# Performance work log

Hardware: AMD Instinct MI355X
Metric: run time of the kernel (lower is better)

The kernel has to match this reference:

```python
import jax, jax.numpy as jnp
import numpy as np

B, S, D, H = 4, 2048, 768, 12
DEPTH = D // H


def setup_inputs() -> dict:
    key = jax.random.key(0)
    ks = jax.random.split(key, 8)
    scale = 1.0 / np.sqrt(D)
    return {
        "v": jax.random.normal(ks[0], (B, S, D), jnp.float32),
        "k": jax.random.normal(ks[1], (B, S, D), jnp.float32),
        "q": jax.random.normal(ks[2], (B, S, D), jnp.float32),
        "wq": jax.random.normal(ks[3], (D, D), jnp.float32) * scale,
        "wk": jax.random.normal(ks[4], (D, D), jnp.float32) * scale,
        "wv": jax.random.normal(ks[5], (D, D), jnp.float32) * scale,
        "wo": jax.random.normal(ks[6], (D, D), jnp.float32) * scale,
        "bo": jax.random.normal(ks[7], (D,), jnp.float32) * 0.01,
    }


def _split_heads(x):
    # [B, S, D] -> [B, H, S, depth]
    return x.reshape(B, S, H, DEPTH).transpose(0, 2, 1, 3)


def reference(v, k, q, wq, wk, wv, wo, bo):
    # nn.Linear(bias=False): y = x @ W.T
    qh = _split_heads(q @ wq.T)
    kh = _split_heads(k @ wk.T)
    vh = _split_heads(v @ wv.T)
    # scaled dot-product attention (mask=None)
    logits = jnp.einsum("bhqd,bhkd->bhqk", qh, kh) / jnp.sqrt(
        jnp.asarray(DEPTH, jnp.float32)
    )
    attn = jax.nn.softmax(logits, axis=-1)  # [B, H, Sq, Sk]
    out = jnp.einsum("bhqk,bhkd->bhqd", attn, vh)
    concat = out.transpose(0, 2, 1, 3).reshape(B, S, D)
    return concat @ wo.T + bo
```

## Files before the change

### kernel.cpp

```cpp
#include <hip/hip_runtime.h>
#include <math.h>

#define BB 4
#define SS 2048
#define DD 768
#define HH 12
#define DEPTH 64
#define M_TOTAL (BB * SS)
#define WSZ (DD * DD)

typedef __attribute__((ext_vector_type(8))) short bf16x8;
typedef __attribute__((ext_vector_type(16))) float f32x16;
typedef __attribute__((ext_vector_type(4))) float f32x4;
typedef __attribute__((ext_vector_type(4))) unsigned short us4;
typedef __attribute__((ext_vector_type(2))) unsigned int u32x2;
typedef __attribute__((ext_vector_type(4))) unsigned int u32x4;

__device__ __forceinline__ unsigned short f2b(float f) {
  unsigned u = __builtin_bit_cast(unsigned, f);
  return (unsigned short)((u + 0x8000u) >> 16);
}

__device__ __forceinline__ unsigned pkrnd(float lo, float hi) {
  unsigned a = __builtin_bit_cast(unsigned, lo) + 0x8000u;
  unsigned b = __builtin_bit_cast(unsigned, hi) + 0x8000u;
  return __builtin_amdgcn_perm(b, a, 0x07060302);
}

__device__ __forceinline__ us4 f2b4(float a, float b, float c, float d) {
  unsigned lo = pkrnd(a, b), hi = pkrnd(c, d);
  us4 t;
  t.x = (unsigned short)lo; t.y = (unsigned short)(lo >> 16);
  t.z = (unsigned short)hi; t.w = (unsigned short)(hi >> 16);
  return t;
}

__device__ __forceinline__ unsigned cvtpk(float a, float b) {
  unsigned d;
  asm("v_cvt_pk_bf16_f32 %0, %1, %2" : "=v"(d) : "v"(a), "v"(b));
  return d;
}

__device__ __forceinline__ u32x2 permswap(unsigned a, unsigned b) {
  auto r = __builtin_amdgcn_permlane32_swap(a, b, false, false);
  u32x2 out;
  out.x = r[0];
  out.y = r[1];
  return out;
}

__device__ __forceinline__ float fexp2(float x) {
  return __builtin_amdgcn_exp2f(x);
}

__device__ __forceinline__ void gl16(const void* g, void* l) {
  __builtin_amdgcn_global_load_lds(
      (const __attribute__((address_space(1))) unsigned int*)g,
      (__attribute__((address_space(3))) unsigned int*)l, 16, 0, 0);
}

__global__ __launch_bounds__(256) void prep(
    const float* __restrict__ s0, const float* __restrict__ s1,
    const float* __restrict__ s2, const float* __restrict__ s3,
    const float* __restrict__ s4, const float* __restrict__ s5,
    const float* __restrict__ s6, unsigned short* __restrict__ d0,
    unsigned short* __restrict__ d1, unsigned short* __restrict__ d2,
    unsigned short* __restrict__ d3, unsigned short* __restrict__ d4,
    unsigned short* __restrict__ d5, unsigned short* __restrict__ d6) {
  const float* s;
  unsigned short* d;
  int n;
  switch (blockIdx.y) {
    case 0: s = s0; d = d0; n = M_TOTAL * DD; break;
    case 1: s = s1; d = d1; n = M_TOTAL * DD; break;
    case 2: s = s2; d = d2; n = M_TOTAL * DD; break;
    case 3: s = s3; d = d3; n = WSZ; break;
    case 4: s = s4; d = d4; n = WSZ; break;
    case 5: s = s5; d = d5; n = WSZ; break;
    default: s = s6; d = d6; n = WSZ; break;
  }
  int idx = (blockIdx.x * 256 + threadIdx.x) * 4;
  if (idx >= n) return;
  float4 f = *(const float4*)(s + idx);
  *(us4*)(d + idx) = f2b4(f.x, f.y, f.z, f.w);
}

__global__ __launch_bounds__(256) void proj_qkv(
    const unsigned short* __restrict__ qb, const unsigned short* __restrict__ kb,
    const unsigned short* __restrict__ vb, const unsigned short* __restrict__ wqb,
    const unsigned short* __restrict__ wkb, const unsigned short* __restrict__ wvb,
    unsigned short* __restrict__ QF, unsigned short* __restrict__ KF,
    unsigned short* __restrict__ VF) {
  const int mode = blockIdx.z;
  const unsigned short* X;
  const unsigned short* W;
  if (mode == 0) { X = qb; W = wqb; }
  else if (mode == 1) { X = kb; W = wkb; }
  else { X = vb; W = wvb; }

  __shared__ __align__(16) char sm[34816];
  unsigned short* As = (unsigned short*)sm;
  unsigned short* Bs = (unsigned short*)(sm + 8192);
  unsigned short* Ts = (unsigned short*)sm;

  const int tid = threadIdx.x;
  const int lane = tid & 63, w_ = tid >> 6;
  const int lr = lane & 15, quad = lane >> 4;
  const int wm = (w_ & 1) * 64, wn = (w_ >> 1) * 64;
  const int lin = blockIdx.y * 64 + blockIdx.x;
  const int nlin = (lin & 7) * 48 + (lin >> 3);
  const int m0 = (nlin / 6) * 128, n0 = (nlin % 6) * 128;
  const int grow = lane >> 2, gcol = (lane & 3) * 8;

  f32x4 acc[4][4];
#pragma unroll
  for (int mt = 0; mt < 4; ++mt)
#pragma unroll
    for (int nt = 0; nt < 4; ++nt) acc[mt][nt] = (f32x4){0.f, 0.f, 0.f, 0.f};

  for (int k0 = 0; k0 < DD; k0 += 32) {
    __syncthreads();
#pragma unroll
    for (int i = 0; i < 2; ++i) {
      int c = 4 * i + w_;
      int row = c * 16 + grow;
      gl16(X + (size_t)(m0 + row) * DD + k0 + gcol, (char*)As + c * 1024);
      gl16(W + (size_t)(n0 + row) * DD + k0 + gcol, (char*)Bs + c * 1024);
    }
    __syncthreads();

    bf16x8 af[4];
#pragma unroll
    for (int mt = 0; mt < 4; ++mt)
      af[mt] = *(const bf16x8*)&As[(wm + 16 * mt + lr) * 32 + 8 * quad];
#pragma unroll
    for (int nt = 0; nt < 4; ++nt) {
      bf16x8 bf = *(const bf16x8*)&Bs[(wn + 16 * nt + lr) * 32 + 8 * quad];
#pragma unroll
      for (int mt = 0; mt < 4; ++mt)
        acc[mt][nt] = __builtin_amdgcn_mfma_f32_16x16x32_bf16(af[mt], bf,
                                                              acc[mt][nt], 0, 0, 0);
    }
  }

  __syncthreads();

  const int b_ = m0 >> 11;
  const int hbase = n0 >> 6;
  const int sgbase = (m0 & 2047) >> 5;

  if (mode < 2) {
    const float osc = (mode == 0) ? 0.18033688011f : 1.0f;
#pragma unroll
    for (int mt = 0; mt < 4; ++mt)
#pragma unroll
      for (int nt = 0; nt < 4; ++nt) {
        int n = wn + 16 * nt + lr;
        int mb = wm + 16 * mt + 4 * quad;
#pragma unroll
        for (int r = 0; r < 4; ++r)
          Ts[(mb + r) * 136 + n] = f2b(acc[mt][nt][r] * osc);
      }
    __syncthreads();
    unsigned short* O = (mode == 0) ? QF : KF;
    const int ks = tid >> 6, lane2 = tid & 63;
    const int mrow = lane2 & 31, hb = lane2 >> 5;
#pragma unroll
    for (int c = 0; c < 8; ++c) {
      int hl = c >> 2, sblk = c & 3;
      int bh = b_ * HH + hbase + hl;
      bf16x8 vv = *(const bf16x8*)&Ts[(sblk * 32 + mrow) * 136 + hl * 64 +
                                      ks * 16 + hb * 8];
      *(bf16x8*)(O + ((size_t)bh * 64 + sgbase + sblk) * 2048 + tid * 8) = vv;
    }
  } else {
#pragma unroll
    for (int mt = 0; mt < 4; ++mt)
#pragma unroll
      for (int nt = 0; nt < 4; ++nt) {
        int n = wn + 16 * nt + lr;
        int mb = wm + 16 * mt + 4 * quad;
        *(us4*)&Ts[n * 136 + mb] =
            f2b4(acc[mt][nt][0], acc[mt][nt][1], acc[mt][nt][2], acc[mt][nt][3]);
      }
    __syncthreads();
    const int ntv = tid >> 7, ks2 = (tid >> 6) & 1, lane2 = tid & 63;
#pragma unroll
    for (int c = 0; c < 8; ++c) {
      int hl = c >> 2, sblk = c & 3;
      int bh = b_ * HH + hbase + hl;
      bf16x8 vv = *(const bf16x8*)&Ts[(hl * 64 + ntv * 32 + (lane2 & 31)) * 136 +
                                      sblk * 32 + ks2 * 16 + (lane2 >> 5) * 8];
      *(bf16x8*)(VF + ((size_t)bh * 64 + sgbase + sblk) * 2048 + tid * 8) = vv;
    }
  }
}

struct KV {
  bf16x8 k[4];
  bf16x8 v[4];
};

__global__ __launch_bounds__(256) void attn(
    const unsigned short* __restrict__ QF, const unsigned short* __restrict__ KF,
    const unsigned short* __restrict__ VF, unsigned short* __restrict__ cc) {
  __shared__ __align__(16) char smem[19200];
  float (*Osh)[64][36] = (float (*)[64][36])smem;
  float (*Ls)[2][32] = (float (*)[2][32])(smem + 18432);
  float (*Linv)[32] = (float (*)[32])(smem + 18944);

  const int tid = threadIdx.x;
  const int lane = tid & 63, w_ = tid >> 6;
  const int wq = w_ & 1, wk = w_ >> 1;
  const int m32 = lane & 31, h = lane >> 5;
  const int lin = blockIdx.y * 32 + blockIdx.x;
  const int nlin = (lin & 7) * 192 + (lin >> 3);
  const int bh = nlin >> 5;
  const int q0 = (nlin & 31) * 64;
  const size_t perbh = (size_t)SS * DEPTH;

  const unsigned short* qfb = QF + (size_t)bh * perbh;
  const unsigned short* kfb = KF + (size_t)bh * perbh + (size_t)wk * 2048 + lane * 8;
  const unsigned short* vfb = VF + (size_t)bh * perbh + (size_t)wk * 2048 + lane * 8;

  bf16x8 qf[4];
  {
    const unsigned short* p = qfb + (size_t)((q0 >> 5) + wq) * 2048 + lane * 8;
#pragma unroll
    for (int ks = 0; ks < 4; ++ks) qf[ks] = *(const bf16x8*)(p + ks * 512);
  }

  f32x16 o[2];
#pragma unroll
  for (int nt = 0; nt < 2; ++nt)
#pragma unroll
    for (int r = 0; r < 16; ++r) o[nt][r] = 0.f;
  float l_lane = 0.f;

#define LOADKV(tile, dst)                                                    \
  do {                                                                       \
    const unsigned short* kp_ = kfb + (size_t)(tile) * 4096;                 \
    const unsigned short* vp_ = vfb + (size_t)(tile) * 4096;                 \
    _Pragma("unroll") for (int x_ = 0; x_ < 4; ++x_) {                       \
      (dst).k[x_] = *(const bf16x8*)(kp_ + x_ * 512);                        \
      (dst).v[x_] = *(const bf16x8*)(vp_ + x_ * 512);                        \
    }                                                                        \
  } while (0)

#define QKCOMP(kv, st)                                                       \
  do {                                                                       \
    _Pragma("unroll") for (int r_ = 0; r_ < 16; ++r_) (st)[r_] = 0.f;        \
    __builtin_amdgcn_s_setprio(1);                                           \
    _Pragma("unroll") for (int ks_ = 0; ks_ < 4; ++ks_)                      \
        (st) = __builtin_amdgcn_mfma_f32_32x32x16_bf16((kv).k[ks_], qf[ks_], \
                                                       (st), 0, 0, 0);       \
    __builtin_amdgcn_s_setprio(0);                                           \
  } while (0)

#define EXPPV(st, kv)                                                        \
  do {                                                                       \
    float e_[16];                                                            \
    _Pragma("unroll") for (int r_ = 0; r_ < 16; ++r_) e_[r_] = fexp2((st)[r_]); \
    _Pragma("unroll") for (int g_ = 0; g_ < 4; ++g_)                         \
        l_lane += (e_[4 * g_ + 0] + e_[4 * g_ + 1]) +                        \
                  (e_[4 * g_ + 2] + e_[4 * g_ + 3]);                         \
    unsigned w00 = cvtpk(e_[0], e_[1]), w01 = cvtpk(e_[2], e_[3]);           \
    unsigned w10 = cvtpk(e_[4], e_[5]), w11 = cvtpk(e_[6], e_[7]);           \
    unsigned w20 = cvtpk(e_[8], e_[9]), w21 = cvtpk(e_[10], e_[11]);         \
    unsigned w30 = cvtpk(e_[12], e_[13]), w31 = cvtpk(e_[14], e_[15]);       \
    u32x2 r0 = permswap(w00, w10);                                           \
    u32x2 r1 = permswap(w01, w11);                                           \
    u32x2 r2 = permswap(w20, w30);                                           \
    u32x2 r3 = permswap(w21, w31);                                           \
    u32x4 paw0, paw1;                                                        \
    paw0.x = r0.x; paw0.y = r1.x; paw0.z = r0.y; paw0.w = r1.y;              \
    paw1.x = r2.x; paw1.y = r3.x; paw1.z = r2.y; paw1.w = r3.y;              \
    bf16x8 pa0 = __builtin_bit_cast(bf16x8, paw0);                           \
    bf16x8 pa1 = __builtin_bit_cast(bf16x8, paw1);                           \
    __builtin_amdgcn_s_setprio(1);                                           \
    o[0] = __builtin_amdgcn_mfma_f32_32x32x16_bf16(pa0, (kv).v[0], o[0],     \
                                                   0, 0, 0);                 \
    o[1] = __builtin_amdgcn_mfma_f32_32x32x16_bf16(pa0, (kv).v[2], o[1],     \
                                                   0, 0, 0);                 \
    o[0] = __builtin_amdgcn_mfma_f32_32x32x16_bf16(pa1, (kv).v[1], o[0],     \
                                                   0, 0, 0);                 \
    o[1] = __builtin_amdgcn_mfma_f32_32x32x16_bf16(pa1, (kv).v[3], o[1],     \
                                                   0, 0, 0);                 \
    __builtin_amdgcn_s_setprio(0);                                           \
  } while (0)

  KV b0, b1;
  f32x16 st0, st1;
  LOADKV(0, b0);
  LOADKV(1, b1);
  for (int t = 0; t < 32; t += 2) {
    QKCOMP(b0, st0);
    QKCOMP(b1, st1);
    EXPPV(st0, b0);
    if (t + 2 < 32) LOADKV(t + 2, b0);
    EXPPV(st1, b1);
    if (t + 3 < 32) LOADKV(t + 3, b1);
  }

  l_lane += __shfl_xor(l_lane, 32);
  if (h == 0) Ls[wq][wk][m32] = l_lane;
  __syncthreads();
  if (wk == 1) {
#pragma unroll
    for (int nt = 0; nt < 2; ++nt)
#pragma unroll
      for (int g = 0; g < 4; ++g) {
        float4 t = make_float4(o[nt][4 * g], o[nt][4 * g + 1], o[nt][4 * g + 2],
                               o[nt][4 * g + 3]);
        *(float4*)&Osh[wq][32 * nt + m32][8 * g + 4 * h] = t;
      }
  } else if (tid < 64) {
    int qq = tid & 31, ww = tid >> 5;
    Linv[ww][qq] = 1.f / (Ls[ww][0][qq] + Ls[ww][1][qq]);
  }
  __syncthreads();
  if (wk == 0) {
    const int b_ = bh / HH, h_ = bh % HH;
#pragma unroll
    for (int g = 0; g < 4; ++g) {
      float4 li = *(const float4*)&Linv[wq][8 * g + 4 * h];
      float lia[4] = {li.x, li.y, li.z, li.w};
#pragma unroll
      for (int nt = 0; nt < 2; ++nt) {
        float4 ot = *(const float4*)&Osh[wq][32 * nt + m32][8 * g + 4 * h];
        float oa[4] = {ot.x, ot.y, ot.z, ot.w};
#pragma unroll
        for (int r = 0; r < 4; ++r) {
          int qg = q0 + 32 * wq + 8 * g + 4 * h + r;
          float val = (o[nt][4 * g + r] + oa[r]) * lia[r];
          cc[((size_t)b_ * SS + qg) * DD + h_ * DEPTH + 32 * nt + m32] = f2b(val);
        }
      }
    }
  }
}

__global__ __launch_bounds__(256) void proj_out(
    const unsigned short* __restrict__ cc, const unsigned short* __restrict__ wob,
    const float* __restrict__ bo, float* __restrict__ out) {
  __shared__ __align__(16) unsigned short As[128 * 32];
  __shared__ __align__(16) unsigned short Bs[128 * 32];

  const int tid = threadIdx.x;
  const int lane = tid & 63, w_ = tid >> 6;
  const int lr = lane & 15, quad = lane >> 4;
  const int wm = (w_ & 1) * 64, wn = (w_ >> 1) * 64;
  const int lin = blockIdx.y * 64 + blockIdx.x;
  const int nlin = (lin & 7) * 48 + (lin >> 3);
  const int m0 = (nlin / 6) * 128, n0 = (nlin % 6) * 128;
  const int grow = lane >> 2, gcol = (lane & 3) * 8;

  f32x4 acc[4][4];
#pragma unroll
  for (int mt = 0; mt < 4; ++mt)
#pragma unroll
    for (int nt = 0; nt < 4; ++nt) acc[mt][nt] = (f32x4){0.f, 0.f, 0.f, 0.f};

  for (int k0 = 0; k0 < DD; k0 += 32) {
    __syncthreads();
#pragma unroll
    for (int i = 0; i < 2; ++i) {
      int c = 4 * i + w_;
      int row = c * 16 + grow;
      gl16(cc + (size_t)(m0 + row) * DD + k0 + gcol, (char*)As + c * 1024);
      gl16(wob + (size_t)(n0 + row) * DD + k0 + gcol, (char*)Bs + c * 1024);
    }
    __syncthreads();

    bf16x8 af[4];
#pragma unroll
    for (int mt = 0; mt < 4; ++mt)
      af[mt] = *(const bf16x8*)&As[(wm + 16 * mt + lr) * 32 + 8 * quad];
#pragma unroll
    for (int nt = 0; nt < 4; ++nt) {
      bf16x8 bf = *(const bf16x8*)&Bs[(wn + 16 * nt + lr) * 32 + 8 * quad];
#pragma unroll
      for (int mt = 0; mt < 4; ++mt)
        acc[mt][nt] = __builtin_amdgcn_mfma_f32_16x16x32_bf16(af[mt], bf,
                                                              acc[mt][nt], 0, 0, 0);
    }
  }

#pragma unroll
  for (int mt = 0; mt < 4; ++mt)
#pragma unroll
    for (int nt = 0; nt < 4; ++nt) {
      int n = n0 + wn + 16 * nt + lr;
      float bias = bo[n];
#pragma unroll
      for (int r = 0; r < 4; ++r) {
        int m = m0 + wm + 16 * mt + 4 * quad + r;
        out[(size_t)m * DD + n] = acc[mt][nt][r] + bias;
      }
    }
}

extern "C" void kernel_launch(void* const* d_in, const int* in_sizes, int n_in,
                              void* d_out, int out_size, void* d_ws,
                              size_t ws_size, hipStream_t stream) {
  const float* v = (const float*)d_in[0];
  const float* k = (const float*)d_in[1];
  const float* q = (const float*)d_in[2];
  const float* wq = (const float*)d_in[3];
  const float* wk = (const float*)d_in[4];
  const float* wv = (const float*)d_in[5];
  const float* wo = (const float*)d_in[6];
  const float* bo = (const float*)d_in[7];
  float* out = (float*)d_out;

  const size_t per = (size_t)BB * HH * SS * DEPTH;
  unsigned short* QF = (unsigned short*)d_ws;
  unsigned short* KF = QF + per;
  unsigned short* VF = KF + per;
  unsigned short* cc = VF + per;
  unsigned short* qb = cc + per;
  unsigned short* kb = qb + per;
  unsigned short* vb = kb + per;
  unsigned short* wqb = vb + per;
  unsigned short* wkb = wqb + WSZ;
  unsigned short* wvb = wkb + WSZ;
  unsigned short* wob = wvb + WSZ;

  dim3 g0(M_TOTAL * DD / 1024, 7);
  prep<<<g0, 256, 0, stream>>>(q, k, v, wq, wk, wv, wo, qb, kb, vb, wqb, wkb,
                               wvb, wob);

  dim3 g1(M_TOTAL / 128, DD / 128, 3);
  proj_qkv<<<g1, 256, 0, stream>>>(qb, kb, vb, wqb, wkb, wvb, QF, KF, VF);

  dim3 g2(SS / 64, BB * HH);
  attn<<<g2, 256, 0, stream>>>(QF, KF, VF, cc);

  dim3 g3(M_TOTAL / 128, DD / 128);
  proj_out<<<g3, 256, 0, stream>>>(cc, wob, bo, out);
}
```

Baseline: 271.0 us.

## Double attention query tile per block and compact prep launch grid

The attention kernel now handles 128 queries per block instead of 64. Each wave keeps two 32-row query fragments, so every K/V tile loaded into registers feeds twice as many MFMAs, which halves K/V global traffic per query. The cost is more registers, shared memory doubled to about 38 KB, and half as many blocks. Separately, the prep conversion kernel moves from a 2D grid, where many blocks exited early for the small weight matrices, to a 1D grid sized exactly to the data, which removes the idle blocks.

Result: slower. 276.7 us (+2.1%).

```diff
diff --git a/kernel.cpp b/kernel.cpp
--- a/kernel.cpp
+++ b/kernel.cpp
@@ -69,18 +69,23 @@
     unsigned short* __restrict__ d5, unsigned short* __restrict__ d6) {
   const float* s;
   unsigned short* d;
-  int n;
-  switch (blockIdx.y) {
-    case 0: s = s0; d = d0; n = M_TOTAL * DD; break;
-    case 1: s = s1; d = d1; n = M_TOTAL * DD; break;
-    case 2: s = s2; d = d2; n = M_TOTAL * DD; break;
-    case 3: s = s3; d = d3; n = WSZ; break;
-    case 4: s = s4; d = d4; n = WSZ; break;
-    case 5: s = s5; d = d5; n = WSZ; break;
-    default: s = s6; d = d6; n = WSZ; break;
-  }
-  int idx = (blockIdx.x * 256 + threadIdx.x) * 4;
-  if (idx >= n) return;
+  int b = blockIdx.x, lb;
+  if (b < 18432) {
+    int mode = b / 6144;
+    lb = b - mode * 6144;
+    if (mode == 0) { s = s0; d = d0; }
+    else if (mode == 1) { s = s1; d = d1; }
+    else { s = s2; d = d2; }
+  } else {
+    int t = b - 18432;
+    int mode = t / 576;
+    lb = t - mode * 576;
+    if (mode == 0) { s = s3; d = d3; }
+    else if (mode == 1) { s = s4; d = d4; }
+    else if (mode == 2) { s = s5; d = d5; }
+    else { s = s6; d = d6; }
+  }
+  int idx = (lb * 256 + threadIdx.x) * 4;
   float4 f = *(const float4*)(s + idx);
   *(us4*)(d + idx) = f2b4(f.x, f.y, f.z, f.w);
 }
@@ -204,38 +209,42 @@
 __global__ __launch_bounds__(256) void attn(
     const unsigned short* __restrict__ QF, const unsigned short* __restrict__ KF,
     const unsigned short* __restrict__ VF, unsigned short* __restrict__ cc) {
-  __shared__ __align__(16) char smem[19200];
-  float (*Osh)[64][36] = (float (*)[64][36])smem;
-  float (*Ls)[2][32] = (float (*)[2][32])(smem + 18432);
-  float (*Linv)[32] = (float (*)[32])(smem + 18944);
+  __shared__ __align__(16) char smem[38400];
+  float (*Osh)[2][64][36] = (float (*)[2][64][36])smem;
+  float (*Ls)[2][2][32] = (float (*)[2][2][32])(smem + 36864);
+  float (*Linv)[2][32] = (float (*)[2][32])(smem + 37888);
 
   const int tid = threadIdx.x;
   const int lane = tid & 63, w_ = tid >> 6;
   const int wq = w_ & 1, wk = w_ >> 1;
   const int m32 = lane & 31, h = lane >> 5;
-  const int lin = blockIdx.y * 32 + blockIdx.x;
-  const int nlin = (lin & 7) * 192 + (lin >> 3);
-  const int bh = nlin >> 5;
-  const int q0 = (nlin & 31) * 64;
+  const int lin = blockIdx.y * 16 + blockIdx.x;
+  const int nlin = (lin & 7) * 96 + (lin >> 3);
+  const int bh = nlin >> 4;
+  const int q0 = (nlin & 15) * 128;
   const size_t perbh = (size_t)SS * DEPTH;
 
   const unsigned short* qfb = QF + (size_t)bh * perbh;
   const unsigned short* kfb = KF + (size_t)bh * perbh + (size_t)wk * 2048 + lane * 8;
   const unsigned short* vfb = VF + (size_t)bh * perbh + (size_t)wk * 2048 + lane * 8;
 
-  bf16x8 qf[4];
+  bf16x8 qf0[4], qf1[4];
   {
-    const unsigned short* p = qfb + (size_t)((q0 >> 5) + wq) * 2048 + lane * 8;
-#pragma unroll
-    for (int ks = 0; ks < 4; ++ks) qf[ks] = *(const bf16x8*)(p + ks * 512);
-  }
-
-  f32x16 o[2];
+    const unsigned short* p0 =
+        qfb + (size_t)((q0 >> 5) + 2 * wq) * 2048 + lane * 8;
+#pragma unroll
+    for (int ks = 0; ks < 4; ++ks) {
+      qf0[ks] = *(const bf16x8*)(p0 + ks * 512);
+      qf1[ks] = *(const bf16x8*)(p0 + 2048 + ks * 512);
+    }
+  }
+
+  f32x16 o0[2], o1[2];
 #pragma unroll
   for (int nt = 0; nt < 2; ++nt)
 #pragma unroll
-    for (int r = 0; r < 16; ++r) o[nt][r] = 0.f;
-  float l_lane = 0.f;
+    for (int r = 0; r < 16; ++r) { o0[nt][r] = 0.f; o1[nt][r] = 0.f; }
+  float l0 = 0.f, l1 = 0.f;
 
 #define LOADKV(tile, dst)                                                    \
   do {                                                                       \
@@ -247,23 +256,13 @@
     }                                                                        \
   } while (0)
 
-#define QKCOMP(kv, st)                                                       \
-  do {                                                                       \
-    _Pragma("unroll") for (int r_ = 0; r_ < 16; ++r_) (st)[r_] = 0.f;        \
-    __builtin_amdgcn_s_setprio(1);                                           \
-    _Pragma("unroll") for (int ks_ = 0; ks_ < 4; ++ks_)                      \
-        (st) = __builtin_amdgcn_mfma_f32_32x32x16_bf16((kv).k[ks_], qf[ks_], \
-                                                       (st), 0, 0, 0);       \
-    __builtin_amdgcn_s_setprio(0);                                           \
-  } while (0)
-
-#define EXPPV(st, kv)                                                        \
+#define EXPPV(st, kv, oo, ll)                                                \
   do {                                                                       \
     float e_[16];                                                            \
     _Pragma("unroll") for (int r_ = 0; r_ < 16; ++r_) e_[r_] = fexp2((st)[r_]); \
     _Pragma("unroll") for (int g_ = 0; g_ < 4; ++g_)                         \
-        l_lane += (e_[4 * g_ + 0] + e_[4 * g_ + 1]) +                        \
-                  (e_[4 * g_ + 2] + e_[4 * g_ + 3]);                         \
+        (ll) += (e_[4 * g_ + 0] + e_[4 * g_ + 1]) +                          \
+                (e_[4 * g_ + 2] + e_[4 * g_ + 3]);                           \
     unsigned w00 = cvtpk(e_[0], e_[1]), w01 = cvtpk(e_[2], e_[3]);           \
     unsigned w10 = cvtpk(e_[4], e_[5]), w11 = cvtpk(e_[6], e_[7]);           \
     unsigned w20 = cvtpk(e_[8], e_[9]), w21 = cvtpk(e_[10], e_[11]);         \
@@ -278,62 +277,93 @@
     bf16x8 pa0 = __builtin_bit_cast(bf16x8, paw0);                           \
     bf16x8 pa1 = __builtin_bit_cast(bf16x8, paw1);                           \
     __builtin_amdgcn_s_setprio(1);                                           \
-    o[0] = __builtin_amdgcn_mfma_f32_32x32x16_bf16(pa0, (kv).v[0], o[0],     \
-                                                   0, 0, 0);                 \
-    o[1] = __builtin_amdgcn_mfma_f32_32x32x16_bf16(pa0, (kv).v[2], o[1],     \
-                                                   0, 0, 0);                 \
-    o[0] = __builtin_amdgcn_mfma_f32_32x32x16_bf16(pa1, (kv).v[1], o[0],     \
-                                                   0, 0, 0);                 \
-    o[1] = __builtin_amdgcn_mfma_f32_32x32x16_bf16(pa1, (kv).v[3], o[1],     \
-                                                   0, 0, 0);                 \
+    (oo)[0] = __builtin_amdgcn_mfma_f32_32x32x16_bf16(pa0, (kv).v[0],        \
+                                                      (oo)[0], 0, 0, 0);     \
+    (oo)[1] = __builtin_amdgcn_mfma_f32_32x32x16_bf16(pa0, (kv).v[2],        \
+                                                      (oo)[1], 0, 0, 0);     \
+    (oo)[0] = __builtin_amdgcn_mfma_f32_32x32x16_bf16(pa1, (kv).v[1],        \
+                                                      (oo)[0], 0, 0, 0);     \
+    (oo)[1] = __builtin_amdgcn_mfma_f32_32x32x16_bf16(pa1, (kv).v[3],        \
+                                                      (oo)[1], 0, 0, 0);     \
     __builtin_amdgcn_s_setprio(0);                                           \
   } while (0)
 
+#define TILE2(kv)                                                            \
+  do {                                                                       \
+    f32x16 st0, st1;                                                         \
+    _Pragma("unroll") for (int r_ = 0; r_ < 16; ++r_) {                      \
+      st0[r_] = 0.f; st1[r_] = 0.f;                                          \
+    }                                                                        \
+    __builtin_amdgcn_s_setprio(1);                                           \
+    _Pragma("unroll") for (int ks_ = 0; ks_ < 4; ++ks_)                      \
+        st0 = __builtin_amdgcn_mfma_f32_32x32x16_bf16((kv).k[ks_], qf0[ks_], \
+                                                      st0, 0, 0, 0);         \
+    _Pragma("unroll") for (int ks_ = 0; ks_ < 4; ++ks_)                      \
+        st1 = __builtin_amdgcn_mfma_f32_32x32x16_bf16((kv).k[ks_], qf1[ks_], \
+                                                      st1, 0, 0, 0);         \
+    __builtin_amdgcn_s_setprio(0);                                           \
+    EXPPV(st0, kv, o0, l0);                                                  \
+    EXPPV(st1, kv, o1, l1);                                                  \
+  } while (0)
+
   KV b0, b1;
-  f32x16 st0, st1;
   LOADKV(0, b0);
   LOADKV(1, b1);
   for (int t = 0; t < 32; t += 2) {
-    QKCOMP(b0, st0);
-    QKCOMP(b1, st1);
-    EXPPV(st0, b0);
+    TILE2(b0);
     if (t + 2 < 32) LOADKV(t + 2, b0);
-    EXPPV(st1, b1);
+    TILE2(b1);
     if (t + 3 < 32) LOADKV(t + 3, b1);
   }
 
-  l_lane += __shfl_xor(l_lane, 32);
-  if (h == 0) Ls[wq][wk][m32] = l_lane;
+  l0 += __shfl_xor(l0, 32);
+  l1 += __shfl_xor(l1, 32);
+  if (h == 0) {
+    Ls[wq][0][wk][m32] = l0;
+    Ls[wq][1][wk][m32] = l1;
+  }
   __syncthreads();
   if (wk == 1) {
 #pragma unroll
     for (int nt = 0; nt < 2; ++nt)
 #pragma unroll
       for (int g = 0; g < 4; ++g) {
-        float4 t = make_float4(o[nt][4 * g], o[nt][4 * g + 1], o[nt][4 * g + 2],
-                               o[nt][4 * g + 3]);
-        *(float4*)&Osh[wq][32 * nt + m32][8 * g + 4 * h] = t;
+        float4 t0 = make_float4(o0[nt][4 * g], o0[nt][4 * g + 1],
+                                o0[nt][4 * g + 2], o0[nt][4 * g + 3]);
+        float4 t1 = make_float4(o1[nt][4 * g], o1[nt][4 * g + 1],
+                                o1[nt][4 * g + 2], o1[nt][4 * g + 3]);
+        *(float4*)&Osh[wq][0][32 * nt + m32][8 * g + 4 * h] = t0;
+        *(float4*)&Osh[wq][1][32 * nt + m32][8 * g + 4 * h] = t1;
       }
-  } else if (tid < 64) {
-    int qq = tid & 31, ww = tid >> 5;
-    Linv[ww][qq] = 1.f / (Ls[ww][0][qq] + Ls[ww][1][qq]);
+  } else {
+    int qq = tid & 31, qg_ = (tid >> 5) & 1, wq_ = tid >> 6;
+    Linv[wq_][qg_][qq] =
+        1.f / (Ls[wq_][qg_][0][qq] + Ls[wq_][qg_][1][qq]);
   }
   __syncthreads();
   if (wk == 0) {
     const int b_ = bh / HH, h_ = bh % HH;
 #pragma unroll
     for (int g = 0; g < 4; ++g) {
-      float4 li = *(const float4*)&Linv[wq][8 * g + 4 * h];
-      float lia[4] = {li.x, li.y, li.z, li.w};
+      float4 li0 = *(const float4*)&Linv[wq][0][8 * g + 4 * h];
+      float4 li1 = *(const float4*)&Linv[wq][1][8 * g + 4 * h];
+      float l0a[4] = {li0.x, li0.y, li0.z, li0.w};
+      float l1a[4] = {li1.x, li1.y, li1.z, li1.w};
 #pragma unroll
       for (int nt = 0; nt < 2; ++nt) {
-        float4 ot = *(const float4*)&Osh[wq][32 * nt + m32][8 * g + 4 * h];
-        float oa[4] = {ot.x, ot.y, ot.z, ot.w};
+        float4 p0 = *(const float4*)&Osh[wq][0][32 * nt + m32][8 * g + 4 * h];
+        float4 p1 = *(const float4*)&Osh[wq][1][32 * nt + m32][8 * g + 4 * h];
+        float o0a[4] = {p0.x, p0.y, p0.z, p0.w};
+        float o1a[4] = {p1.x, p1.y, p1.z, p1.w};
 #pragma unroll
         for (int r = 0; r < 4; ++r) {
-          int qg = q0 + 32 * wq + 8 * g + 4 * h + r;
-          float val = (o[nt][4 * g + r] + oa[r]) * lia[r];
-          cc[((size_t)b_ * SS + qg) * DD + h_ * DEPTH + 32 * nt + m32] = f2b(val);
+          int qbase = q0 + 64 * wq + 8 * g + 4 * h + r;
+          float v0 = (o0[nt][4 * g + r] + o0a[r]) * l0a[r];
+          float v1 = (o1[nt][4 * g + r] + o1a[r]) * l1a[r];
+          cc[((size_t)b_ * SS + qbase) * DD + h_ * DEPTH + 32 * nt + m32] =
+              f2b(v0);
+          cc[((size_t)b_ * SS + qbase + 32) * DD + h_ * DEPTH + 32 * nt + m32] =
+              f2b(v1);
         }
       }
     }
@@ -426,14 +456,13 @@
   unsigned short* wvb = wkb + WSZ;
   unsigned short* wob = wvb + WSZ;
 
-  dim3 g0(M_TOTAL * DD / 1024, 7);
-  prep<<<g0, 256, 0, stream>>>(q, k, v, wq, wk, wv, wo, qb, kb, vb, wqb, wkb,
-                               wvb, wob);
+  prep<<<dim3(20736), 256, 0, stream>>>(q, k, v, wq, wk, wv, wo, qb, kb, vb,
+                                        wqb, wkb, wvb, wob);
 
   dim3 g1(M_TOTAL / 128, DD / 128, 3);
   proj_qkv<<<g1, 256, 0, stream>>>(qb, kb, vb, wqb, wkb, wvb, QF, KF, VF);
 
-  dim3 g2(SS / 64, BB * HH);
+  dim3 g2(SS / 128, BB * HH);
   attn<<<g2, 256, 0, stream>>>(QF, KF, VF, cc);
 
   dim3 g3(M_TOTAL / 128, DD / 128);
```

## Fuse fp32-to-bf16 conversion of q/k/v into the QKV projection GEMM

Applied to the files above, without the earlier changes.

The prep kernel no longer converts the large q/k/v activations to bf16. It now converts only the four weight matrices, using a flattened 1D grid. The QKV projection kernel instead loads fp32 activation rows directly, rounds them to bf16 in registers and writes them to shared memory, while weights still use async global-to-LDS loads. This removes a full write and re-read of three bf16 activation copies. In exchange, the GEMM reads fp32 (twice the bytes) and redoes each conversion once for every N-tile column (6 times), with synchronous register staging in place of async LDS loads.

Result: slower. 293.0 us (+8.1%).

```diff
diff --git a/kernel.cpp b/kernel.cpp
--- a/kernel.cpp
+++ b/kernel.cpp
@@ -62,41 +62,33 @@
 __global__ __launch_bounds__(256) void prep(
     const float* __restrict__ s0, const float* __restrict__ s1,
     const float* __restrict__ s2, const float* __restrict__ s3,
-    const float* __restrict__ s4, const float* __restrict__ s5,
-    const float* __restrict__ s6, unsigned short* __restrict__ d0,
-    unsigned short* __restrict__ d1, unsigned short* __restrict__ d2,
-    unsigned short* __restrict__ d3, unsigned short* __restrict__ d4,
-    unsigned short* __restrict__ d5, unsigned short* __restrict__ d6) {
+    unsigned short* __restrict__ d0, unsigned short* __restrict__ d1,
+    unsigned short* __restrict__ d2, unsigned short* __restrict__ d3) {
+  int b = blockIdx.x;
+  int mode = b / 576, lb = b - mode * 576;
   const float* s;
   unsigned short* d;
-  int n;
-  switch (blockIdx.y) {
-    case 0: s = s0; d = d0; n = M_TOTAL * DD; break;
-    case 1: s = s1; d = d1; n = M_TOTAL * DD; break;
-    case 2: s = s2; d = d2; n = M_TOTAL * DD; break;
-    case 3: s = s3; d = d3; n = WSZ; break;
-    case 4: s = s4; d = d4; n = WSZ; break;
-    case 5: s = s5; d = d5; n = WSZ; break;
-    default: s = s6; d = d6; n = WSZ; break;
-  }
-  int idx = (blockIdx.x * 256 + threadIdx.x) * 4;
-  if (idx >= n) return;
+  if (mode == 0) { s = s0; d = d0; }
+  else if (mode == 1) { s = s1; d = d1; }
+  else if (mode == 2) { s = s2; d = d2; }
+  else { s = s3; d = d3; }
+  int idx = (lb * 256 + threadIdx.x) * 4;
   float4 f = *(const float4*)(s + idx);
   *(us4*)(d + idx) = f2b4(f.x, f.y, f.z, f.w);
 }
 
 __global__ __launch_bounds__(256) void proj_qkv(
-    const unsigned short* __restrict__ qb, const unsigned short* __restrict__ kb,
-    const unsigned short* __restrict__ vb, const unsigned short* __restrict__ wqb,
+    const float* __restrict__ qf32, const float* __restrict__ kf32,
+    const float* __restrict__ vf32, const unsigned short* __restrict__ wqb,
     const unsigned short* __restrict__ wkb, const unsigned short* __restrict__ wvb,
     unsigned short* __restrict__ QF, unsigned short* __restrict__ KF,
     unsigned short* __restrict__ VF) {
   const int mode = blockIdx.z;
-  const unsigned short* X;
+  const float* X;
   const unsigned short* W;
-  if (mode == 0) { X = qb; W = wqb; }
-  else if (mode == 1) { X = kb; W = wkb; }
-  else { X = vb; W = wvb; }
+  if (mode == 0) { X = qf32; W = wqb; }
+  else if (mode == 1) { X = kf32; W = wkb; }
+  else { X = vf32; W = wvb; }
 
   __shared__ __align__(16) char sm[34816];
   unsigned short* As = (unsigned short*)sm;
@@ -111,6 +103,7 @@
   const int nlin = (lin & 7) * 48 + (lin >> 3);
   const int m0 = (nlin / 6) * 128, n0 = (nlin % 6) * 128;
   const int grow = lane >> 2, gcol = (lane & 3) * 8;
+  const int arow = tid >> 1, acb = (tid & 1) * 16;
 
   f32x4 acc[4][4];
 #pragma unroll
@@ -118,15 +111,27 @@
 #pragma unroll
     for (int nt = 0; nt < 4; ++nt) acc[mt][nt] = (f32x4){0.f, 0.f, 0.f, 0.f};
 
+  const float* arow_base = X + (size_t)(m0 + arow) * DD + acb;
+
   for (int k0 = 0; k0 < DD; k0 += 32) {
+    float4 av0 = *(const float4*)(arow_base + k0);
+    float4 av1 = *(const float4*)(arow_base + k0 + 4);
+    float4 av2 = *(const float4*)(arow_base + k0 + 8);
+    float4 av3 = *(const float4*)(arow_base + k0 + 12);
     __syncthreads();
 #pragma unroll
     for (int i = 0; i < 2; ++i) {
       int c = 4 * i + w_;
       int row = c * 16 + grow;
-      gl16(X + (size_t)(m0 + row) * DD + k0 + gcol, (char*)As + c * 1024);
       gl16(W + (size_t)(n0 + row) * DD + k0 + gcol, (char*)Bs + c * 1024);
     }
+    u32x4 p0, p1;
+    p0.x = pkrnd(av0.x, av0.y); p0.y = pkrnd(av0.z, av0.w);
+    p0.z = pkrnd(av1.x, av1.y); p0.w = pkrnd(av1.z, av1.w);
+    p1.x = pkrnd(av2.x, av2.y); p1.y = pkrnd(av2.z, av2.w);
+    p1.z = pkrnd(av3.x, av3.y); p1.w = pkrnd(av3.z, av3.w);
+    *(u32x4*)&As[arow * 32 + acb] = p0;
+    *(u32x4*)&As[arow * 32 + acb + 8] = p1;
     __syncthreads();
 
     bf16x8 af[4];
@@ -418,20 +423,15 @@
   unsigned short* KF = QF + per;
   unsigned short* VF = KF + per;
   unsigned short* cc = VF + per;
-  unsigned short* qb = cc + per;
-  unsigned short* kb = qb + per;
-  unsigned short* vb = kb + per;
-  unsigned short* wqb = vb + per;
+  unsigned short* wqb = cc + per;
   unsigned short* wkb = wqb + WSZ;
   unsigned short* wvb = wkb + WSZ;
   unsigned short* wob = wvb + WSZ;
 
-  dim3 g0(M_TOTAL * DD / 1024, 7);
-  prep<<<g0, 256, 0, stream>>>(q, k, v, wq, wk, wv, wo, qb, kb, vb, wqb, wkb,
-                               wvb, wob);
+  prep<<<dim3(2304), 256, 0, stream>>>(wq, wk, wv, wo, wqb, wkb, wvb, wob);
 
   dim3 g1(M_TOTAL / 128, DD / 128, 3);
-  proj_qkv<<<g1, 256, 0, stream>>>(qb, kb, vb, wqb, wkb, wvb, QF, KF, VF);
+  proj_qkv<<<g1, 256, 0, stream>>>(q, k, v, wqb, wkb, wvb, QF, KF, VF);
 
   dim3 g2(SS / 64, BB * HH);
   attn<<<g2, 256, 0, stream>>>(QF, KF, VF, cc);
```
